# Kernel tuning notes

Hardware: AMD Instinct MI355X
Metric: run time of the kernel (lower is better)

The kernel has to match this reference:

```python
import jax, jax.numpy as jnp
import numpy as np

NUM_HEADS = 12


def setup_inputs() -> dict:
    key = jax.random.key(0)
    k1, k2, k3 = jax.random.split(key, 3)
    B, N, C = 2, 2048, 768
    x = jax.random.normal(k1, (B, N, C), dtype=jnp.float32)
    # torch nn.Linear weights: [out_features, in_features]
    w_qkv = jax.random.normal(k2, (3 * C, C), dtype=jnp.float32) * (C ** -0.5)
    w_mlp = jax.random.normal(k3, (C, C), dtype=jnp.float32) * (C ** -0.5)
    b_mlp = jnp.zeros((C,), dtype=jnp.float32)
    return {"x": x, "w_qkv": w_qkv, "w_mlp": w_mlp, "b_mlp": b_mlp}


def reference(x, w_qkv, w_mlp, b_mlp):
    B, N, C = x.shape
    H = NUM_HEADS
    hd = C // H
    scale = hd ** -0.5
    # qkv linear (no bias), then the module's reshape: [B,N,H,3,hd]
    qkv = (x @ w_qkv.T).reshape(B, N, H, 3, hd)
    # permute(3,0,2,1,4) -> q,k,v each [B,H,N,hd]
    q = jnp.transpose(qkv[:, :, :, 0, :], (0, 2, 1, 3))
    k = jnp.transpose(qkv[:, :, :, 1, :], (0, 2, 1, 3))
    v = jnp.transpose(qkv[:, :, :, 2, :], (0, 2, 1, 3))
    attn = jax.nn.softmax(jnp.einsum('bhqd,bhkd->bhqk', q, k) * scale, axis=-1)
    out = jnp.einsum('bhqk,bhkd->bhqd', attn, v)          # [B,H,N,hd]
    out = jnp.transpose(out, (0, 2, 1, 3)).reshape(B, N, C)
    return out @ w_mlp.T + b_mlp
```

## Files before the change

kernel.cpp:

```cpp
#include <hip/hip_runtime.h>
#include <math.h>

typedef unsigned short u16;
typedef unsigned int   u32;
typedef __attribute__((ext_vector_type(8))) short s8v;
typedef __attribute__((ext_vector_type(2))) unsigned int u32x2;
typedef __attribute__((ext_vector_type(4))) float f4v;

#define NHEADS 12
#define SEQ 2048
#define CD 768
#define BB 2
#define QKVD 2304
#define CEXP 0.18033688f
#define DEFER_THR 44.0f

__device__ inline u16 f2bf(float f) {
    union { float f; unsigned u; } v; v.f = f;
    unsigned r = v.u + 0x7FFFu + ((v.u >> 16) & 1u);
    return (u16)(r >> 16);
}
__device__ inline u32 cvtpk_bf16(float lo, float hi) {
    u32 r;
    asm("v_cvt_pk_bf16_f32 %0, %1, %2" : "=v"(r) : "v"(lo), "v"(hi));
    return r;
}
__device__ inline float exp2_fast(float x) {
    float r;
    asm("v_exp_f32 %0, %1" : "=v"(r) : "v"(x));
    return r;
}
__device__ inline float max3f(float a, float b, float c) {
    float r;
    asm("v_max3_f32 %0, %1, %2, %3" : "=v"(r) : "v"(a), "v"(b), "v"(c));
    return r;
}

#define GLOAD16(SRC, DST) __builtin_amdgcn_global_load_lds(                 \
    (const __attribute__((address_space(1))) void*)(SRC),                   \
    (__attribute__((address_space(3))) void*)(DST), 16, 0, 0)

#define SW(r, c) ((((r) << 6) + (c)) ^ (((r) & 7) << 3))

__global__ __launch_bounds__(256)
void cvt3_kernel(const float* __restrict__ a, u16* __restrict__ oa, int na,
                 const float* __restrict__ b, u16* __restrict__ ob, int nb,
                 const float* __restrict__ c, u16* __restrict__ oc) {
    const int i = (blockIdx.x * 256 + threadIdx.x) * 8;
    const float* src; u16* dst;
    if (i < na)           { src = a + i;            dst = oa + i; }
    else if (i < na + nb) { src = b + (i - na);     dst = ob + (i - na); }
    else                  { src = c + (i - na - nb); dst = oc + (i - na - nb); }
    const float4 x = *(const float4*)src;
    const float4 y = *(const float4*)(src + 4);
    s8v o;
    o[0] = (short)f2bf(x.x); o[1] = (short)f2bf(x.y);
    o[2] = (short)f2bf(x.z); o[3] = (short)f2bf(x.w);
    o[4] = (short)f2bf(y.x); o[5] = (short)f2bf(y.y);
    o[6] = (short)f2bf(y.z); o[7] = (short)f2bf(y.w);
    *(s8v*)dst = o;
}

template<int BN, bool OUT_BF16, bool BIAS>
__global__ __launch_bounds__(256)
void gemm_bf16(const u16* __restrict__ A, const u16* __restrict__ W,
               const float* __restrict__ bias, void* __restrict__ Cout,
               int M, int N, int K) {
    constexpr int NF = BN / 32;
    __shared__ u16 As[8192];
    __shared__ u16 Bs[BN * 64];
    const int tid = threadIdx.x;
    const int l  = tid & 63, w = tid >> 6;
    const int wr = w >> 1, wc = w & 1;
    const int lq = l & 15, lg = l >> 4;
    const int rowBase = blockIdx.y << 7, colBase = blockIdx.x * BN;

    f4v acc[4][NF];
    #pragma unroll
    for (int m = 0; m < 4; ++m)
        #pragma unroll
        for (int n = 0; n < NF; ++n)
            #pragma unroll
            for (int r = 0; r < 4; ++r) acc[m][n][r] = 0.f;

    const int chunk = l & 7;
    const int r8    = l >> 3;

    for (int kb = 0; kb < K; kb += 64) {
        __syncthreads();
        #pragma unroll
        for (int j = 0; j < 4; ++j) {
            const int rowA = (w << 5) + (j << 3) + r8;
            const int sc   = (chunk ^ (rowA & 7)) << 3;
            GLOAD16(A + (size_t)(rowBase + rowA) * K + kb + sc,
                    &As[(w << 11) + (j << 9)]);
        }
        #pragma unroll
        for (int j = 0; j < NF; ++j) {
            const int rowB = w * (BN / 4) + (j << 3) + r8;
            const int sc   = (chunk ^ (rowB & 7)) << 3;
            GLOAD16(W + (size_t)(colBase + rowB) * K + kb + sc,
                    &Bs[w * (BN * 16) + (j << 9)]);
        }
        __syncthreads();
        #pragma unroll
        for (int h = 0; h < 2; ++h) {
            const int kc = (h << 5) + (lg << 3);
            s8v af[4], bf[NF];
            #pragma unroll
            for (int m = 0; m < 4; ++m)
                af[m] = *(const s8v*)&As[SW((wr << 6) + (m << 4) + lq, kc)];
            #pragma unroll
            for (int n = 0; n < NF; ++n)
                bf[n] = *(const s8v*)&Bs[SW(wc * (BN / 2) + (n << 4) + lq, kc)];
            #pragma unroll
            for (int m = 0; m < 4; ++m)
                #pragma unroll
                for (int n = 0; n < NF; ++n)
                    acc[m][n] = __builtin_amdgcn_mfma_f32_16x16x32_bf16(
                        af[m], bf[n], acc[m][n], 0, 0, 0);
        }
    }

    #pragma unroll
    for (int m = 0; m < 4; ++m)
        #pragma unroll
        for (int r = 0; r < 4; ++r) {
            const int row = rowBase + (wr << 6) + (m << 4) + (lg << 2) + r;
            #pragma unroll
            for (int n = 0; n < NF; ++n) {
                const int col = colBase + wc * (BN / 2) + (n << 4) + lq;
                float v = acc[m][n][r];
                if (BIAS) v += bias[col];
                if (OUT_BF16) ((u16*)Cout)[(size_t)row * N + col] = f2bf(v);
                else        ((float*)Cout)[(size_t)row * N + col] = v;
            }
        }
}

__global__ __launch_bounds__(256)
void vtrans_kernel(const u16* __restrict__ qkvb, u16* __restrict__ vT) {
    __shared__ u16 T[64][66];
    const int bh = blockIdx.y;
    const int tt = blockIdx.x;
    const int b = bh / NHEADS, h = bh % NHEADS;
    const int r  = threadIdx.x >> 2;
    const int dc = (threadIdx.x & 3) << 4;
    const u16* src = qkvb + (size_t)(b * SEQ + tt * 64 + r) * QKVD
                   + h * 192 + 128 + dc;
    *(s8v*)&T[r][dc]     = *(const s8v*)(src);
    *(s8v*)&T[r][dc + 8] = *(const s8v*)(src + 8);
    __syncthreads();
    const int d  = threadIdx.x >> 2;
    const int tc = (threadIdx.x & 3) << 4;
    s8v o0, o1;
    #pragma unroll
    for (int j = 0; j < 8; ++j) {
        o0[j] = (short)T[tc + j][d];
        o1[j] = (short)T[tc + 8 + j][d];
    }
    u16* dst = vT + ((size_t)bh * 64 + d) * SEQ + tt * 64 + tc;
    *(s8v*)dst = o0;
    *(s8v*)(dst + 8) = o1;
}

__global__ __launch_bounds__(512)
void attn_mfma(const u16* __restrict__ qkv, const u16* __restrict__ vT,
               u16* __restrict__ outb) {
    __shared__ u16 SL[40960];
    const int tid = threadIdx.x;
    const int l = tid & 63, w = tid >> 6;
    const int g = w >> 2, wl = w & 3;
    const int lq = l & 15, lg = l >> 4;
    const int q0 = blockIdx.x << 6;
    const int bh = blockIdx.y;
    const int b = bh / NHEADS, h = bh % NHEADS;
    const u16* base = qkv + (size_t)b * SEQ * QKVD + h * 192;
    const u16* vbh  = vT + (size_t)bh * 64 * SEQ;
    u16* QP = SL + 32768;
    float* Of32 = (float*)(SL + 16384);
    float* Msh  = (float*)(SL + 32768);
    float* Lsh  = Msh + 64;

    const int kv0 = g << 10;

    u32 koff[2], voff[2], kdst[2], vdst[2];
    {
        const int cs = l & 7;
        #pragma unroll
        for (int i = 0; i < 2; ++i) {
            const int row = (wl << 4) + (i << 3) + (l >> 3);
            koff[i] = (u32)(row * QKVD + 64 + ((cs ^ (row & 7)) << 3));
            voff[i] = (u32)(row * SEQ  +      ((cs ^ (row & 7)) << 3));
            kdst[i] = (u32)((g << 14) + (wl << 10) + (i << 9));
            vdst[i] = (u32)((g << 14) + 8192 + (wl << 10) + (i << 9));
        }
    }

    {
        const u16* sbK = base + (size_t)kv0 * QKVD;
        const u16* sbV = vbh + kv0;
        #pragma unroll
        for (int i = 0; i < 2; ++i) {
            GLOAD16(sbK + koff[i], &SL[kdst[i]]);
            GLOAD16(sbV + voff[i], &SL[vdst[i]]);
        }
    }
    {
        const s8v q1 = *(const s8v*)(base + (size_t)(q0 + l) * QKVD + (w << 3));
        *(s8v*)&QP[SW(l, w << 3)] = q1;
    }
    __syncthreads();
    s8v qf[2];
    #pragma unroll
    for (int h2 = 0; h2 < 2; ++h2)
        qf[h2] = *(const s8v*)&QP[SW((wl << 4) + lq, (h2 << 5) + (lg << 3))];

    s8v onesf;
    {
        const short o = (lq == 0) ? (short)0x3F80 : (short)0;
        #pragma unroll
        for (int e = 0; e < 8; ++e) onesf[e] = o;
    }
    f4v fz;
    #pragma unroll
    for (int r = 0; r < 4; ++r) fz[r] = 0.f;

    f4v oacc[4], osum;
    #pragma unroll
    for (int db = 0; db < 4; ++db)
        #pragma unroll
        for (int r = 0; r < 4; ++r) oacc[db][r] = 0.f;
    #pragma unroll
    for (int r = 0; r < 4; ++r) osum[r] = 0.f;
    float mrun = -3.0e38f;

    for (int t = 0; t < 16; ++t) {
        const int par = t & 1;
        const u16* Kc = SL + (g << 14) + (par << 12);
        const u16* Vc = SL + (g << 14) + 8192 + (par << 12);

        if (t < 15) {
            const u16* sbK = base + (size_t)(kv0 + (t + 1) * 64) * QKVD;
            const u16* sbV = vbh + kv0 + (t + 1) * 64;
            const u32 pb = (u32)((par ^ 1) << 12);
            #pragma unroll
            for (int i = 0; i < 2; ++i) {
                GLOAD16(sbK + koff[i], &SL[kdst[i] + pb]);
                GLOAD16(sbV + voff[i], &SL[vdst[i] + pb]);
            }
        }

        float p[16];
        __builtin_amdgcn_s_setprio(1);
        #pragma unroll
        for (int kb = 0; kb < 4; ++kb) {
            const s8v k0 = *(const s8v*)&Kc[SW((kb << 4) + lq, (lg << 3))];
            const s8v k1 = *(const s8v*)&Kc[SW((kb << 4) + lq, 32 + (lg << 3))];
            f4v z;
            z = __builtin_amdgcn_mfma_f32_16x16x32_bf16(k0, qf[0], fz, 0, 0, 0);
            z = __builtin_amdgcn_mfma_f32_16x16x32_bf16(k1, qf[1], z, 0, 0, 0);
            #pragma unroll
            for (int r = 0; r < 4; ++r) p[(kb << 2) + r] = z[r];
        }
        __builtin_amdgcn_s_setprio(0);

        float m1_ = max3f(p[0], p[1], p[2]);
        float m2_ = max3f(p[3], p[4], p[5]);
        float m3_ = max3f(p[6], p[7], p[8]);
        float m4_ = max3f(p[9], p[10], p[11]);
        float m5_ = max3f(p[12], p[13], p[14]);
        float mx  = fmaxf(max3f(m1_, m2_, p[15]), max3f(m3_, m4_, m5_));
        if (!__all(mx <= mrun + DEFER_THR)) {
            mx = fmaxf(mx, __shfl_xor(mx, 16));
            mx = fmaxf(mx, __shfl_xor(mx, 32));
            const float mn = fmaxf(mrun, mx);
            const float al = exp2_fast((mrun - mn) * CEXP);
            mrun = mn;
            float ar[4];
            #pragma unroll
            for (int r = 0; r < 4; ++r) ar[r] = __shfl(al, (lg << 2) + r);
            #pragma unroll
            for (int db = 0; db < 4; ++db)
                #pragma unroll
                for (int r = 0; r < 4; ++r) oacc[db][r] *= ar[r];
            #pragma unroll
            for (int r = 0; r < 4; ++r) osum[r] *= ar[r];
        }
        const float mC = -mrun * CEXP;
        #pragma unroll
        for (int i = 0; i < 16; ++i) p[i] = exp2_fast(fmaf(p[i], CEXP, mC));

        #pragma unroll
        for (int kb = 0; kb < 4; ++kb) {
            u32x2 pw;
            pw[0] = cvtpk_bf16(p[(kb << 2) + 0], p[(kb << 2) + 1]);
            pw[1] = cvtpk_bf16(p[(kb << 2) + 2], p[(kb << 2) + 3]);
            *(u32x2*)&QP[SW((w << 4) + lq, (kb << 4) + (lg << 2))] = pw;
        }
        const s8v pf0 = *(const s8v*)&QP[SW((w << 4) + lq, (lg << 3))];
        const s8v pf1 = *(const s8v*)&QP[SW((w << 4) + lq, 32 + (lg << 3))];

        __builtin_amdgcn_s_setprio(1);
        #pragma unroll
        for (int db = 0; db < 4; ++db) {
            const s8v v0 = *(const s8v*)&Vc[SW((db << 4) + lq, (lg << 3))];
            const s8v v1 = *(const s8v*)&Vc[SW((db << 4) + lq, 32 + (lg << 3))];
            oacc[db] = __builtin_amdgcn_mfma_f32_16x16x32_bf16(pf0, v0, oacc[db], 0, 0, 0);
            oacc[db] = __builtin_amdgcn_mfma_f32_16x16x32_bf16(pf1, v1, oacc[db], 0, 0, 0);
        }
        osum = __builtin_amdgcn_mfma_f32_16x16x32_bf16(pf0, onesf, osum, 0, 0, 0);
        osum = __builtin_amdgcn_mfma_f32_16x16x32_bf16(pf1, onesf, osum, 0, 0, 0);
        __builtin_amdgcn_s_setprio(0);

        __syncthreads();
    }

    if (g == 1) {
        if (lg == 0) Msh[(wl << 4) + lq] = mrun;
        if (lq == 0) {
            #pragma unroll
            for (int r = 0; r < 4; ++r)
                Lsh[(wl << 4) + (lg << 2) + r] = osum[r];
        }
        #pragma unroll
        for (int db = 0; db < 4; ++db)
            #pragma unroll
            for (int r = 0; r < 4; ++r)
                Of32[(((wl << 4) + (lg << 2) + r) << 6) + (db << 4) + lq] =
                    oacc[db][r];
    }
    __syncthreads();
    if (g == 0) {
        #pragma unroll
        for (int r = 0; r < 4; ++r) {
            const int rowq = (wl << 4) + (lg << 2) + r;
            const float m0r = __shfl(mrun, (lg << 2) + r);
            const float l0r = __shfl(osum[r], l & 48);
            const float m1r = Msh[rowq];
            const float l1r = Lsh[rowq];
            const float M   = fmaxf(m0r, m1r);
            const float w0  = exp2_fast((m0r - M) * CEXP);
            const float w1  = exp2_fast((m1r - M) * CEXP);
            const float inv = 1.f / (l0r * w0 + l1r * w1);
            const float a0 = w0 * inv, a1 = w1 * inv;
            const size_t row = (size_t)b * SEQ + q0 + rowq;
            #pragma unroll
            for (int db = 0; db < 4; ++db) {
                const float o1 = Of32[(rowq << 6) + (db << 4) + lq];
                outb[row * CD + h * 64 + (db << 4) + lq] =
                    f2bf(oacc[db][r] * a0 + o1 * a1);
            }
        }
    }
}

extern "C" void kernel_launch(void* const* d_in, const int* in_sizes, int n_in,
                              void* d_out, int out_size, void* d_ws, size_t ws_size,
                              hipStream_t stream) {
    const float* x     = (const float*)d_in[0];
    const float* w_qkv = (const float*)d_in[1];
    const float* w_mlp = (const float*)d_in[2];
    const float* b_mlp = (const float*)d_in[3];
    float* out = (float*)d_out;

    const int NX  = BB * SEQ * CD;
    const int NWQ = QKVD * CD;
    const int NWM = CD * CD;
    const int NQK = BB * SEQ * QKVD;
    const int NAT = BB * SEQ * CD;
    u16* xb    = (u16*)d_ws;
    u16* wqkvb = xb + NX;
    u16* wmlpb = wqkvb + NWQ;
    u16* qkvb  = wmlpb + NWM;
    u16* attnb = qkvb + NQK;
    u16* vTb   = attnb + NAT;

    cvt3_kernel<<<(NX + NWQ + NWM) / 2048, 256, 0, stream>>>(
        x, xb, NX, w_qkv, wqkvb, NWQ, w_mlp, wmlpb);

    const int M = BB * SEQ;
    {
        dim3 grid(QKVD / 128, M / 128);
        gemm_bf16<128, true, false><<<grid, 256, 0, stream>>>(xb, wqkvb, nullptr,
                                                              qkvb, M, QKVD, CD);
    }
    {
        dim3 grid(SEQ / 64, BB * NHEADS);
        vtrans_kernel<<<grid, 256, 0, stream>>>(qkvb, vTb);
    }
    {
        dim3 grid(SEQ / 64, BB * NHEADS);
        attn_mfma<<<grid, 512, 0, stream>>>(qkvb, vTb, attnb);
    }
    {
        dim3 grid(CD / 64, M / 128);
        gemm_bf16<64, false, true><<<grid, 256, 0, stream>>>(attnb, wmlpb, b_mlp,
                                                             out, M, CD, CD);
    }
}
```

Measured before the change: 93.11 us.

## Single-buffer attention K/V tiles and swizzle block order for XCD locality

The attention kernel drops K/V double buffering, which cuts LDS from about 80KB to 48KB per block so more blocks can be resident per CU. The next K and V tiles are now prefetched into the same buffer right after their last use, separated by extra barriers. The GEMMs and attention also move to 1D grids with an XCD-aware swizzle, so neighbouring tiles (sharing A rows or heads) land on the same XCD for L2 reuse. The risk is less load/compute overlap within a block and two more barriers per iteration.

```diff
diff --git a/kernel.cpp b/kernel.cpp
--- a/kernel.cpp
+++ b/kernel.cpp
@@ -61,7 +61,7 @@
     *(s8v*)dst = o;
 }
 
-template<int BN, bool OUT_BF16, bool BIAS>
+template<int BN, int NBX, bool OUT_BF16, bool BIAS>
 __global__ __launch_bounds__(256)
 void gemm_bf16(const u16* __restrict__ A, const u16* __restrict__ W,
                const float* __restrict__ bias, void* __restrict__ Cout,
@@ -73,7 +73,12 @@
     const int l  = tid & 63, w = tid >> 6;
     const int wr = w >> 1, wc = w & 1;
     const int lq = l & 15, lg = l >> 4;
-    const int rowBase = blockIdx.y << 7, colBase = blockIdx.x * BN;
+
+    const int fid = blockIdx.x;
+    const int cpx = gridDim.x >> 3;
+    const int swz = (fid & 7) * cpx + (fid >> 3);
+    const int rowBase = (swz / NBX) << 7;
+    const int colBase = (swz % NBX) * BN;
 
     f4v acc[4][NF];
     #pragma unroll
@@ -167,19 +172,22 @@
 __global__ __launch_bounds__(512)
 void attn_mfma(const u16* __restrict__ qkv, const u16* __restrict__ vT,
                u16* __restrict__ outb) {
-    __shared__ u16 SL[40960];
+    __shared__ u16 SL[24576];
     const int tid = threadIdx.x;
     const int l = tid & 63, w = tid >> 6;
     const int g = w >> 2, wl = w & 3;
     const int lq = l & 15, lg = l >> 4;
-    const int q0 = blockIdx.x << 6;
-    const int bh = blockIdx.y;
+
+    const int fid = blockIdx.x;
+    const int swz = (fid & 7) * 96 + (fid >> 3);
+    const int q0 = (swz & 31) << 6;
+    const int bh = swz >> 5;
     const int b = bh / NHEADS, h = bh % NHEADS;
     const u16* base = qkv + (size_t)b * SEQ * QKVD + h * 192;
     const u16* vbh  = vT + (size_t)bh * 64 * SEQ;
-    u16* QP = SL + 32768;
-    float* Of32 = (float*)(SL + 16384);
-    float* Msh  = (float*)(SL + 32768);
+    u16* QP = SL + 16384;
+    float* Of32 = (float*)(SL + 8192);
+    float* Msh  = (float*)(SL + 16384);
     float* Lsh  = Msh + 64;
 
     const int kv0 = g << 10;
@@ -192,8 +200,8 @@
             const int row = (wl << 4) + (i << 3) + (l >> 3);
             koff[i] = (u32)(row * QKVD + 64 + ((cs ^ (row & 7)) << 3));
             voff[i] = (u32)(row * SEQ  +      ((cs ^ (row & 7)) << 3));
-            kdst[i] = (u32)((g << 14) + (wl << 10) + (i << 9));
-            vdst[i] = (u32)((g << 14) + 8192 + (wl << 10) + (i << 9));
+            kdst[i] = (u32)((g << 13) + (wl << 10) + (i << 9));
+            vdst[i] = (u32)((g << 13) + 4096 + (wl << 10) + (i << 9));
         }
     }
 
@@ -235,21 +243,11 @@
     for (int r = 0; r < 4; ++r) osum[r] = 0.f;
     float mrun = -3.0e38f;
 
+    const u16* Kc = SL + (g << 13);
+    const u16* Vc = Kc + 4096;
+
     for (int t = 0; t < 16; ++t) {
-        const int par = t & 1;
-        const u16* Kc = SL + (g << 14) + (par << 12);
-        const u16* Vc = SL + (g << 14) + 8192 + (par << 12);
-
-        if (t < 15) {
-            const u16* sbK = base + (size_t)(kv0 + (t + 1) * 64) * QKVD;
-            const u16* sbV = vbh + kv0 + (t + 1) * 64;
-            const u32 pb = (u32)((par ^ 1) << 12);
-            #pragma unroll
-            for (int i = 0; i < 2; ++i) {
-                GLOAD16(sbK + koff[i], &SL[kdst[i] + pb]);
-                GLOAD16(sbV + voff[i], &SL[vdst[i] + pb]);
-            }
-        }
+        __syncthreads();
 
         float p[16];
         __builtin_amdgcn_s_setprio(1);
@@ -264,6 +262,14 @@
             for (int r = 0; r < 4; ++r) p[(kb << 2) + r] = z[r];
         }
         __builtin_amdgcn_s_setprio(0);
+
+        __syncthreads();
+        if (t < 15) {
+            const u16* sbK = base + (size_t)(kv0 + (t + 1) * 64) * QKVD;
+            #pragma unroll
+            for (int i = 0; i < 2; ++i)
+                GLOAD16(sbK + koff[i], &SL[kdst[i]]);
+        }
 
         float m1_ = max3f(p[0], p[1], p[2]);
         float m2_ = max3f(p[3], p[4], p[5]);
@@ -314,6 +320,12 @@
         __builtin_amdgcn_s_setprio(0);
 
         __syncthreads();
+        if (t < 15) {
+            const u16* sbV = vbh + kv0 + (t + 1) * 64;
+            #pragma unroll
+            for (int i = 0; i < 2; ++i)
+                GLOAD16(sbV + voff[i], &SL[vdst[i]]);
+        }
     }
 
     if (g == 1) {
@@ -381,21 +393,18 @@
 
     const int M = BB * SEQ;
     {
-        dim3 grid(QKVD / 128, M / 128);
-        gemm_bf16<128, true, false><<<grid, 256, 0, stream>>>(xb, wqkvb, nullptr,
-                                                              qkvb, M, QKVD, CD);
+        gemm_bf16<128, 18, true, false><<<576, 256, 0, stream>>>(
+            xb, wqkvb, nullptr, qkvb, M, QKVD, CD);
     }
     {
         dim3 grid(SEQ / 64, BB * NHEADS);
         vtrans_kernel<<<grid, 256, 0, stream>>>(qkvb, vTb);
     }
     {
-        dim3 grid(SEQ / 64, BB * NHEADS);
-        attn_mfma<<<grid, 512, 0, stream>>>(qkvb, vTb, attnb);
-    }
-    {
-        dim3 grid(CD / 64, M / 128);
-        gemm_bf16<64, false, true><<<grid, 256, 0, stream>>>(attnb, wmlpb, b_mlp,
-                                                             out, M, CD, CD);
-    }
-}
+        attn_mfma<<<768, 512, 0, stream>>>(qkvb, vTb, attnb);
+    }
+    {
+        gemm_bf16<64, 12, false, true><<<384, 256, 0, stream>>>(
+            attnb, wmlpb, b_mlp, out, M, CD, CD);
+    }
+}
```

Result: faster. 91.01 us (-2.3%).
